# Performance work log

Measured on AMD Instinct MI355X. Metric: run time of the kernel, lower is better.

Reference implementation:

```python
import jax, jax.numpy as jnp
import numpy as np

DIM = 768
NUM_HEADS = 12
HEAD_DIM = DIM // NUM_HEADS
HIDDEN = int(DIM * 0.5)  # 384, per Block: hidden_features = int(dim * 0.5)
SCALE = HEAD_DIM ** 0.5  # NOTE: source multiplies by sqrt(head_dim) (qk_scale=None path)


def setup_inputs() -> dict:
    key = jax.random.key(0)
    ks = jax.random.split(key, 10)
    s = 0.02
    return {
        "x": jax.random.normal(ks[0], (8, 1024, DIM), dtype=jnp.float32),
        "ln1_w": jnp.ones((DIM,), jnp.float32),
        "ln1_b": jnp.zeros((DIM,), jnp.float32),
        "ln2_w": jnp.ones((DIM,), jnp.float32),
        "ln2_b": jnp.zeros((DIM,), jnp.float32),
        "w_qkv": jax.random.normal(ks[1], (DIM, 3 * DIM), jnp.float32) * s,  # no bias (qkv_bias=None)
        "w_proj": jax.random.normal(ks[2], (DIM, DIM), jnp.float32) * s,    # no bias (qkv_bias=None)
        "w_fc1": jax.random.normal(ks[3], (DIM, HIDDEN), jnp.float32) * s,
        "b_fc1": jnp.zeros((HIDDEN,), jnp.float32),
        "w_fc2": jax.random.normal(ks[4], (HIDDEN, DIM), jnp.float32) * s,
        "b_fc2": jnp.zeros((DIM,), jnp.float32),
    }


def _layernorm(x, w, b, eps=1e-5):
    mu = jnp.mean(x, axis=-1, keepdims=True)
    var = jnp.mean(jnp.square(x - mu), axis=-1, keepdims=True)
    return (x - mu) * jax.lax.rsqrt(var + eps) * w + b


def reference(x, ln1_w, ln1_b, ln2_w, ln2_b, w_qkv, w_proj, w_fc1, b_fc1, w_fc2, b_fc2):
    B, N, C = x.shape
    # --- attention branch (pre-norm) ---
    h = _layernorm(x, ln1_w, ln1_b)
    qkv = h @ w_qkv  # [B,N,3C]
    qkv = qkv.reshape(B, N, 3, NUM_HEADS, HEAD_DIM)
    q = jnp.transpose(qkv[:, :, 0], (0, 2, 1, 3))  # [B,H,N,D]
    k = jnp.transpose(qkv[:, :, 1], (0, 2, 1, 3))
    v = jnp.transpose(qkv[:, :, 2], (0, 2, 1, 3))
    attn = jnp.einsum("bhnd,bhmd->bhnm", q, k) * SCALE
    attn = jax.nn.softmax(attn, axis=-1)
    out = jnp.einsum("bhnm,bhmd->bhnd", attn, v)
    out = jnp.transpose(out, (0, 2, 1, 3)).reshape(B, N, C)
    x = x + out @ w_proj
    # --- MLP branch (pre-norm) ---
    h = _layernorm(x, ln2_w, ln2_b)
    h = jax.nn.gelu(h @ w_fc1 + b_fc1, approximate=False)
    x = x + (h @ w_fc2 + b_fc2)
    return x
```

## Files before the change

kernel.cpp:

```cpp
#include <hip/hip_runtime.h>
#include <hip/hip_bf16.h>
#include <math.h>

#define DIM 768
#define NHEAD 12
#define HD 64
#define HIDDEN 384
#define BATCH 8
#define SEQ 1024
#define ROWS (BATCH*SEQ)
#define CHUNKB 4
#define CHUNKR (CHUNKB*SEQ)

typedef short bf16x8 __attribute__((ext_vector_type(8)));
typedef short bf16x4 __attribute__((ext_vector_type(4)));
typedef float f32x4 __attribute__((ext_vector_type(4)));
typedef unsigned short u16;
typedef unsigned int u32;

__device__ __forceinline__ u16 f2bs(float f) {
    unsigned int u = __float_as_uint(f);
    unsigned int r = (u + 0x7FFFu + ((u >> 16) & 1u)) >> 16;
    return (u16)r;
}

__device__ __forceinline__ u32 packbf2(float a, float b) {
    __hip_bfloat162 h = __float22bfloat162_rn(make_float2(a, b));
    u32 r;
    __builtin_memcpy(&r, &h, 4);
    return r;
}

__device__ __forceinline__ void gld16(const u16* g, u16* l) {
    __builtin_amdgcn_global_load_lds(
        (const __attribute__((address_space(1))) unsigned int*)g,
        (__attribute__((address_space(3))) unsigned int*)l, 16, 0, 0);
}

__global__ __launch_bounds__(256) void wtrans(const float* __restrict__ W,
                                              u16* __restrict__ Wt, int K, int N) {
    __shared__ float tile[32][33];
    int n0 = blockIdx.x * 32, k0 = blockIdx.y * 32;
    int tx = threadIdx.x & 31, ty = threadIdx.x >> 5;
#pragma unroll
    for (int i = 0; i < 4; i++)
        tile[ty + i * 8][tx] = W[(long)(k0 + ty + i * 8) * N + n0 + tx];
    __syncthreads();
#pragma unroll
    for (int i = 0; i < 4; i++)
        Wt[(long)(n0 + ty + i * 8) * K + k0 + tx] = f2bs(tile[tx][ty + i * 8]);
}

__global__ __launch_bounds__(256) void lnorm(const float* __restrict__ X,
                                             const float* __restrict__ w,
                                             const float* __restrict__ b,
                                             u16* __restrict__ Y) {
    int row = blockIdx.x;
    const float* xr = X + (long)row * DIM;
    int t = threadIdx.x;
    float v0 = xr[t], v1 = xr[t + 256], v2 = xr[t + 512];
    float s = v0 + v1 + v2;
    float s2 = v0 * v0 + v1 * v1 + v2 * v2;
    for (int off = 1; off < 64; off <<= 1) {
        s  += __shfl_xor(s,  off, 64);
        s2 += __shfl_xor(s2, off, 64);
    }
    __shared__ float ss[4], ss2[4];
    int wid = t >> 6;
    if ((t & 63) == 0) { ss[wid] = s; ss2[wid] = s2; }
    __syncthreads();
    s  = ss[0] + ss[1] + ss[2] + ss[3];
    s2 = ss2[0] + ss2[1] + ss2[2] + ss2[3];
    float mu = s * (1.0f / DIM);
    float var = s2 * (1.0f / DIM) - mu * mu;
    float rstd = rsqrtf(var + 1e-5f);
    u16* yr = Y + (long)row * DIM;
    yr[t]       = f2bs((v0 - mu) * rstd * w[t]       + b[t]);
    yr[t + 256] = f2bs((v1 - mu) * rstd * w[t + 256] + b[t + 256]);
    yr[t + 512] = f2bs((v2 - mu) * rstd * w[t + 512] + b[t + 512]);
}

template <int BM, int BN, int EPI>
__global__ __launch_bounds__(256) void gemm_bt(const u16* __restrict__ A,
                                               const u16* __restrict__ Bt,
                                               int M, int N, int K,
                                               u16* __restrict__ Cb,
                                               float* __restrict__ Cf,
                                               const float* __restrict__ resid,
                                               const float* __restrict__ bias) {
    constexpr int MB = BM / 32, NB = BN / 32;
    __shared__ u16 As[BM * 64];
    __shared__ u16 Bs[BN * 64];
    int m0 = blockIdx.y * BM;
    int n0 = blockIdx.x * BN;
    int t = threadIdx.x;
    int lane = t & 63, w = t >> 6;
    int quad = lane >> 4, l16 = lane & 15;
    int wr = w >> 1, wc = w & 1;
    int lr = lane >> 3, lc = lane & 7;
    int sc = (lc ^ lr) * 8;
    int x7 = l16 & 7;

    f32x4 acc[MB][NB];
#pragma unroll
    for (int mb = 0; mb < MB; mb++)
#pragma unroll
        for (int nb = 0; nb < NB; nb++) acc[mb][nb] = (f32x4){0.f, 0.f, 0.f, 0.f};

    for (int kt = 0; kt < K; kt += 64) {
        __syncthreads();
#pragma unroll
        for (int i = 0; i < BM / 32; i++) {
            int rb = i * 32 + w * 8;
            gld16(&A[(long)(m0 + rb + lr) * K + kt + sc], &As[rb * 64]);
        }
#pragma unroll
        for (int i = 0; i < BN / 32; i++) {
            int rb = i * 32 + w * 8;
            gld16(&Bt[(long)(n0 + rb + lr) * K + kt + sc], &Bs[rb * 64]);
        }
        __syncthreads();
#pragma unroll
        for (int kh = 0; kh < 2; kh++) {
            bf16x8 af[MB], bfr[NB];
#pragma unroll
            for (int mb = 0; mb < MB; mb++)
                af[mb] = *(const bf16x8*)&As[(wr * (BM / 2) + mb * 16 + l16) * 64 +
                                             (((kh * 4 + quad) ^ x7) * 8)];
#pragma unroll
            for (int nb = 0; nb < NB; nb++)
                bfr[nb] = *(const bf16x8*)&Bs[(wc * (BN / 2) + nb * 16 + l16) * 64 +
                                              (((kh * 4 + quad) ^ x7) * 8)];
#pragma unroll
            for (int mb = 0; mb < MB; mb++)
#pragma unroll
                for (int nb = 0; nb < NB; nb++)
                    acc[mb][nb] = __builtin_amdgcn_mfma_f32_16x16x32_bf16(af[mb], bfr[nb], acc[mb][nb], 0, 0, 0);
        }
    }

    int mbase = m0 + wr * (BM / 2), nbase = n0 + wc * (BN / 2);
#pragma unroll
    for (int mb = 0; mb < MB; mb++)
#pragma unroll
        for (int nb = 0; nb < NB; nb++) {
            int r0 = mbase + mb * 16 + quad * 4;
            int c = nbase + nb * 16 + l16;
#pragma unroll
            for (int r = 0; r < 4; r++) {
                float v = acc[mb][nb][r];
                long idx = (long)(r0 + r) * N + c;
                if (EPI == 0) {
                    Cb[idx] = f2bs(v);
                } else if (EPI == 1) {
                    Cf[idx] = resid[idx] + v;
                } else if (EPI == 2) {
                    float xg = v + bias[c];
                    Cb[idx] = f2bs(xg * 0.5f * (1.0f + erff(xg * 0.70710678118f)));
                } else {
                    Cf[idx] = resid[idx] + v + bias[c];
                }
            }
        }
}

__global__ __launch_bounds__(256, 4) void attn(const u16* __restrict__ QKV, u16* __restrict__ O) {
    __shared__ u16 Ks[2][64 * 64];
    __shared__ u16 Vs[2][64 * 72];
    int lin = blockIdx.x;
    int cpx = gridDim.x >> 3;
    int l = (lin & 7) * cpx + (lin >> 3);
    int q0 = (l & 15) * 64;
    int hb = l >> 4;
    int h = hb % NHEAD;
    int b = hb / NHEAD;
    int t = threadIdx.x;
    int lane = t & 63, w = t >> 6;
    int quad = lane >> 4, l16 = lane & 15;
    int x7 = l16 & 7;

    const long rs = 3 * DIM;
    const u16* base = QKV + (long)b * SEQ * rs;

    bf16x8 qf0, qf1;
    {
        int qrow = q0 + w * 16 + l16;
        qf0 = *(const bf16x8*)&base[(long)qrow * rs + h * 64 + quad * 8];
        qf1 = *(const bf16x8*)&base[(long)qrow * rs + h * 64 + 32 + quad * 8];
    }

    f32x4 o[4];
#pragma unroll
    for (int dt = 0; dt < 4; dt++) o[dt] = (f32x4){0.f, 0.f, 0.f, 0.f};
    float m_run = -1e30f;
    float l_run = 0.f;
    const float L2E8 = 11.54156032f;

    int lr = lane >> 3, lc = lane & 7;
    int sc = (lc ^ lr) * 8;
    const u16* kA = &base[(long)(w * 16 + lr) * rs + DIM + h * 64 + sc];
    const u16* kB = kA + (long)8 * rs;
    int vc = t & 31, vo = t >> 5;
    const u16* vptr = &base[(long)(2 * vc) * rs + 2 * DIM + h * 64 + vo * 8];
    const long kstep = (long)64 * rs;

    bf16x8 vp0, vp1;
    gld16(kA, &Ks[0][(w * 16) * 64]);
    gld16(kB, &Ks[0][(w * 16 + 8) * 64]);
    kA += kstep; kB += kstep;
    vp0 = *(const bf16x8*)&vptr[0];
    vp1 = *(const bf16x8*)&vptr[rs];
    vptr += kstep;
#pragma unroll
    for (int j = 0; j < 8; j++) {
        u32 pk = (u32)(u16)vp0[j] | ((u32)(u16)vp1[j] << 16);
        *(u32*)&Vs[0][(vo * 8 + j) * 72 + 2 * vc] = pk;
    }
    vp0 = *(const bf16x8*)&vptr[0];
    vp1 = *(const bf16x8*)&vptr[rs];
    vptr += kstep;
    __syncthreads();

    for (int it = 0; it < SEQ / 64; it++) {
        int cur = it & 1;
        if (it < SEQ / 64 - 1) {
            int nb = cur ^ 1;
            gld16(kA, &Ks[nb][(w * 16) * 64]);
            gld16(kB, &Ks[nb][(w * 16 + 8) * 64]);
            kA += kstep; kB += kstep;
#pragma unroll
            for (int j = 0; j < 8; j++) {
                u32 pk = (u32)(u16)vp0[j] | ((u32)(u16)vp1[j] << 16);
                *(u32*)&Vs[nb][(vo * 8 + j) * 72 + 2 * vc] = pk;
            }
            if (it < SEQ / 64 - 2) {
                vp0 = *(const bf16x8*)&vptr[0];
                vp1 = *(const bf16x8*)&vptr[rs];
                vptr += kstep;
            }
        }

        f32x4 s[4];
#pragma unroll
        for (int jb = 0; jb < 4; jb++) {
            int row = jb * 16 + l16;
            bf16x8 kf0 = *(const bf16x8*)&Ks[cur][row * 64 + ((quad ^ x7) * 8)];
            bf16x8 kf1 = *(const bf16x8*)&Ks[cur][row * 64 + (((4 + quad) ^ x7) * 8)];
            f32x4 z = (f32x4){0.f, 0.f, 0.f, 0.f};
            z = __builtin_amdgcn_mfma_f32_16x16x32_bf16(kf0, qf0, z, 0, 0, 0);
            z = __builtin_amdgcn_mfma_f32_16x16x32_bf16(kf1, qf1, z, 0, 0, 0);
            s[jb] = z;
        }

        f32x4 mx = __builtin_elementwise_max(__builtin_elementwise_max(s[0], s[1]),
                                             __builtin_elementwise_max(s[2], s[3]));
        float m1 = fmaxf(fmaxf(mx[0], mx[1]), fmaxf(mx[2], mx[3]));
        m1 = fmaxf(m1, __shfl_xor(m1, 16, 64));
        m1 = fmaxf(m1, __shfl_xor(m1, 32, 64));

        float mn = m_run;
        int resc = __any(m1 > mn + 1.0f);
        if (resc) mn = fmaxf(mn, m1);
        float mn8 = mn * L2E8;
        f32x4 cmul = {L2E8, L2E8, L2E8, L2E8};
        f32x4 cadd = {-mn8, -mn8, -mn8, -mn8};
#pragma unroll
        for (int jb = 0; jb < 4; jb++) {
            f32x4 e = s[jb] * cmul + cadd;
            e[0] = exp2f(e[0]); e[1] = exp2f(e[1]);
            e[2] = exp2f(e[2]); e[3] = exp2f(e[3]);
            s[jb] = e;
        }
        f32x4 sv = (s[0] + s[1]) + (s[2] + s[3]);
        float rsum = (sv[0] + sv[1]) + (sv[2] + sv[3]);
        rsum += __shfl_xor(rsum, 16, 64);
        rsum += __shfl_xor(rsum, 32, 64);

        if (resc) {
            float alpha = exp2f((m_run - mn) * L2E8);
            m_run = mn;
            float a0 = __shfl(alpha, quad * 4 + 0, 16);
            float a1 = __shfl(alpha, quad * 4 + 1, 16);
            float a2 = __shfl(alpha, quad * 4 + 2, 16);
            float a3 = __shfl(alpha, quad * 4 + 3, 16);
#pragma unroll
            for (int dt = 0; dt < 4; dt++) {
                o[dt][0] *= a0; o[dt][1] *= a1;
                o[dt][2] *= a2; o[dt][3] *= a3;
            }
            l_run = l_run * alpha + rsum;
        } else {
            l_run += rsum;
        }

#pragma unroll
        for (int jb = 0; jb < 4; jb++) {
            union { u32 u[2]; bf16x4 v; } pc;
            pc.u[0] = packbf2(s[jb][0], s[jb][1]);
            pc.u[1] = packbf2(s[jb][2], s[jb][3]);
            bf16x4 pf = pc.v;
#pragma unroll
            for (int dt = 0; dt < 4; dt++) {
                bf16x4 vf = *(const bf16x4*)&Vs[cur][(dt * 16 + l16) * 72 + jb * 16 + quad * 4];
                o[dt] = __builtin_amdgcn_mfma_f32_16x16x16bf16_1k(pf, vf, o[dt], 0, 0, 0);
            }
        }

        if (it < SEQ / 64 - 1) __syncthreads();
    }

    {
        float l0 = __shfl(l_run, quad * 4 + 0, 16);
        float l1 = __shfl(l_run, quad * 4 + 1, 16);
        float l2 = __shfl(l_run, quad * 4 + 2, 16);
        float l3 = __shfl(l_run, quad * 4 + 3, 16);
        u16* orow = O + ((long)(b * SEQ + q0 + w * 16)) * DIM + h * 64;
#pragma unroll
        for (int dt = 0; dt < 4; dt++) {
            u32 p01 = packbf2(o[dt][0] / l0, o[dt][1] / l1);
            u32 p23 = packbf2(o[dt][2] / l2, o[dt][3] / l3);
            int cidx = dt * 16 + l16;
            orow[(long)(quad * 4 + 0) * DIM + cidx] = (u16)p01;
            orow[(long)(quad * 4 + 1) * DIM + cidx] = (u16)(p01 >> 16);
            orow[(long)(quad * 4 + 2) * DIM + cidx] = (u16)p23;
            orow[(long)(quad * 4 + 3) * DIM + cidx] = (u16)(p23 >> 16);
        }
    }
}

extern "C" void kernel_launch(void* const* d_in, const int* in_sizes, int n_in,
                              void* d_out, int out_size, void* d_ws, size_t ws_size,
                              hipStream_t stream) {
    const float* x     = (const float*)d_in[0];
    const float* ln1w  = (const float*)d_in[1];
    const float* ln1b  = (const float*)d_in[2];
    const float* ln2w  = (const float*)d_in[3];
    const float* ln2b  = (const float*)d_in[4];
    const float* wqkv  = (const float*)d_in[5];
    const float* wproj = (const float*)d_in[6];
    const float* wfc1  = (const float*)d_in[7];
    const float* bfc1  = (const float*)d_in[8];
    const float* wfc2  = (const float*)d_in[9];
    const float* bfc2  = (const float*)d_in[10];
    float* out = (float*)d_out;

    char* ws = (char*)d_ws;
    size_t off = 0;
    auto alloc = [&](size_t bytes) {
        void* p = ws + off;
        off = (off + bytes + 255) & ~(size_t)255;
        return p;
    };
    u16* wt_qkv  = (u16*)alloc((size_t)3 * DIM * DIM * 2);
    u16* wt_proj = (u16*)alloc((size_t)DIM * DIM * 2);
    u16* wt_fc1  = (u16*)alloc((size_t)HIDDEN * DIM * 2);
    u16* wt_fc2  = (u16*)alloc((size_t)DIM * HIDDEN * 2);
    u16* hbuf    = (u16*)alloc((size_t)ROWS * DIM * 2);
    u16* gbuf    = (u16*)alloc((size_t)ROWS * HIDDEN * 2);
    size_t qkv_bytes = (size_t)ROWS * 3 * DIM * 2;
    u16* qkvfull = (off + qkv_bytes + 1024 <= ws_size) ? (u16*)alloc(qkv_bytes) : nullptr;

    wtrans<<<dim3(3 * DIM / 32, DIM / 32), 256, 0, stream>>>(wqkv, wt_qkv, DIM, 3 * DIM);
    wtrans<<<dim3(DIM / 32, DIM / 32), 256, 0, stream>>>(wproj, wt_proj, DIM, DIM);
    wtrans<<<dim3(HIDDEN / 32, DIM / 32), 256, 0, stream>>>(wfc1, wt_fc1, DIM, HIDDEN);
    wtrans<<<dim3(DIM / 32, HIDDEN / 32), 256, 0, stream>>>(wfc2, wt_fc2, HIDDEN, DIM);

    lnorm<<<ROWS, 256, 0, stream>>>(x, ln1w, ln1b, hbuf);

    if (qkvfull) {
        gemm_bt<128, 128, 0><<<dim3(3 * DIM / 128, ROWS / 128), 256, 0, stream>>>(
            hbuf, wt_qkv, ROWS, 3 * DIM, DIM, qkvfull, nullptr, nullptr, nullptr);
        attn<<<(SEQ / 64) * NHEAD * BATCH, 256, 0, stream>>>(qkvfull, hbuf);
    } else {
        u16* qd = (u16*)d_out;
        for (int c = 0; c < ROWS / CHUNKR; c++) {
            const u16* hA = hbuf + (size_t)c * CHUNKR * DIM;
            gemm_bt<128, 128, 0><<<dim3(3 * DIM / 128, CHUNKR / 128), 256, 0, stream>>>(
                hA, wt_qkv, CHUNKR, 3 * DIM, DIM, qd, nullptr, nullptr, nullptr);
            attn<<<(SEQ / 64) * NHEAD * CHUNKB, 256, 0, stream>>>(
                qd, hbuf + (size_t)c * CHUNKR * DIM);
        }
    }

    gemm_bt<128, 64, 1><<<dim3(DIM / 64, ROWS / 128), 256, 0, stream>>>(
        hbuf, wt_proj, ROWS, DIM, DIM, nullptr, out, x, nullptr);

    lnorm<<<ROWS, 256, 0, stream>>>(out, ln2w, ln2b, hbuf);

    gemm_bt<64, 64, 2><<<dim3(HIDDEN / 64, ROWS / 64), 256, 0, stream>>>(
        hbuf, wt_fc1, ROWS, HIDDEN, DIM, gbuf, nullptr, nullptr, bfc1);

    gemm_bt<128, 64, 3><<<dim3(DIM / 64, ROWS / 128), 256, 0, stream>>>(
        gbuf, wt_fc2, ROWS, DIM, HIDDEN, nullptr, out, out, bfc2);
}
```

Measured before the change: 293.2 us.

## Use 128-query attention blocks with 8 waves sharing K/V tiles; fuse weight transposes

The attention kernel now launches 512-thread blocks, each covering 128 query rows with 8 waves. Every K/V tile staged in shared memory is reused by twice as many queries, and each thread loads half as much per tile. The four weight-transpose launches are merged into one kernel that picks its matrix from the block index, saving launch overhead. The trade-off is half as many attention blocks and a higher occupancy target (launch bounds 512,6), which may constrain registers.

```diff
diff --git a/kernel.cpp b/kernel.cpp
--- a/kernel.cpp
+++ b/kernel.cpp
@@ -37,10 +37,18 @@
         (__attribute__((address_space(3))) unsigned int*)l, 16, 0, 0);
 }
 
-__global__ __launch_bounds__(256) void wtrans(const float* __restrict__ W,
-                                              u16* __restrict__ Wt, int K, int N) {
+__global__ __launch_bounds__(256) void wtrans4(const float* __restrict__ W0, u16* __restrict__ T0,
+                                               const float* __restrict__ W1, u16* __restrict__ T1,
+                                               const float* __restrict__ W2, u16* __restrict__ T2,
+                                               const float* __restrict__ W3, u16* __restrict__ T3) {
     __shared__ float tile[32][33];
-    int n0 = blockIdx.x * 32, k0 = blockIdx.y * 32;
+    int id = blockIdx.x;
+    const float* W; u16* T; int K, N, nt;
+    if (id < 1728)      {            W = W0; T = T0; K = 768; N = 2304; nt = 72; }
+    else if (id < 2304) { id -= 1728; W = W1; T = T1; K = 768; N = 768;  nt = 24; }
+    else if (id < 2592) { id -= 2304; W = W2; T = T2; K = 768; N = 384;  nt = 12; }
+    else                { id -= 2592; W = W3; T = T3; K = 384; N = 768;  nt = 24; }
+    int n0 = (id % nt) * 32, k0 = (id / nt) * 32;
     int tx = threadIdx.x & 31, ty = threadIdx.x >> 5;
 #pragma unroll
     for (int i = 0; i < 4; i++)
@@ -48,7 +56,7 @@
     __syncthreads();
 #pragma unroll
     for (int i = 0; i < 4; i++)
-        Wt[(long)(n0 + ty + i * 8) * K + k0 + tx] = f2bs(tile[tx][ty + i * 8]);
+        T[(long)(n0 + ty + i * 8) * K + k0 + tx] = f2bs(tile[tx][ty + i * 8]);
 }
 
 __global__ __launch_bounds__(256) void lnorm(const float* __restrict__ X,
@@ -164,14 +172,14 @@
         }
 }
 
-__global__ __launch_bounds__(256, 4) void attn(const u16* __restrict__ QKV, u16* __restrict__ O) {
+__global__ __launch_bounds__(512, 6) void attn(const u16* __restrict__ QKV, u16* __restrict__ O) {
     __shared__ u16 Ks[2][64 * 64];
     __shared__ u16 Vs[2][64 * 72];
     int lin = blockIdx.x;
     int cpx = gridDim.x >> 3;
     int l = (lin & 7) * cpx + (lin >> 3);
-    int q0 = (l & 15) * 64;
-    int hb = l >> 4;
+    int q0 = (l & 7) * 128;
+    int hb = l >> 3;
     int h = hb % NHEAD;
     int b = hb / NHEAD;
     int t = threadIdx.x;
@@ -198,26 +206,24 @@
 
     int lr = lane >> 3, lc = lane & 7;
     int sc = (lc ^ lr) * 8;
-    const u16* kA = &base[(long)(w * 16 + lr) * rs + DIM + h * 64 + sc];
-    const u16* kB = kA + (long)8 * rs;
+    const u16* kA = &base[(long)(w * 8 + lr) * rs + DIM + h * 64 + sc];
     int vc = t & 31, vo = t >> 5;
-    const u16* vptr = &base[(long)(2 * vc) * rs + 2 * DIM + h * 64 + vo * 8];
+    const u16* vptr = &base[(long)(2 * vc) * rs + 2 * DIM + h * 64 + vo * 4];
     const long kstep = (long)64 * rs;
 
-    bf16x8 vp0, vp1;
-    gld16(kA, &Ks[0][(w * 16) * 64]);
-    gld16(kB, &Ks[0][(w * 16 + 8) * 64]);
-    kA += kstep; kB += kstep;
-    vp0 = *(const bf16x8*)&vptr[0];
-    vp1 = *(const bf16x8*)&vptr[rs];
+    bf16x4 vp0, vp1;
+    gld16(kA, &Ks[0][(w * 8) * 64]);
+    kA += kstep;
+    vp0 = *(const bf16x4*)&vptr[0];
+    vp1 = *(const bf16x4*)&vptr[rs];
     vptr += kstep;
 #pragma unroll
-    for (int j = 0; j < 8; j++) {
+    for (int j = 0; j < 4; j++) {
         u32 pk = (u32)(u16)vp0[j] | ((u32)(u16)vp1[j] << 16);
-        *(u32*)&Vs[0][(vo * 8 + j) * 72 + 2 * vc] = pk;
-    }
-    vp0 = *(const bf16x8*)&vptr[0];
-    vp1 = *(const bf16x8*)&vptr[rs];
+        *(u32*)&Vs[0][(vo * 4 + j) * 72 + 2 * vc] = pk;
+    }
+    vp0 = *(const bf16x4*)&vptr[0];
+    vp1 = *(const bf16x4*)&vptr[rs];
     vptr += kstep;
     __syncthreads();
 
@@ -225,17 +231,16 @@
         int cur = it & 1;
         if (it < SEQ / 64 - 1) {
             int nb = cur ^ 1;
-            gld16(kA, &Ks[nb][(w * 16) * 64]);
-            gld16(kB, &Ks[nb][(w * 16 + 8) * 64]);
-            kA += kstep; kB += kstep;
-#pragma unroll
-            for (int j = 0; j < 8; j++) {
+            gld16(kA, &Ks[nb][(w * 8) * 64]);
+            kA += kstep;
+#pragma unroll
+            for (int j = 0; j < 4; j++) {
                 u32 pk = (u32)(u16)vp0[j] | ((u32)(u16)vp1[j] << 16);
-                *(u32*)&Vs[nb][(vo * 8 + j) * 72 + 2 * vc] = pk;
+                *(u32*)&Vs[nb][(vo * 4 + j) * 72 + 2 * vc] = pk;
             }
             if (it < SEQ / 64 - 2) {
-                vp0 = *(const bf16x8*)&vptr[0];
-                vp1 = *(const bf16x8*)&vptr[rs];
+                vp0 = *(const bf16x4*)&vptr[0];
+                vp1 = *(const bf16x4*)&vptr[rs];
                 vptr += kstep;
             }
         }
@@ -360,24 +365,22 @@
     size_t qkv_bytes = (size_t)ROWS * 3 * DIM * 2;
     u16* qkvfull = (off + qkv_bytes + 1024 <= ws_size) ? (u16*)alloc(qkv_bytes) : nullptr;
 
-    wtrans<<<dim3(3 * DIM / 32, DIM / 32), 256, 0, stream>>>(wqkv, wt_qkv, DIM, 3 * DIM);
-    wtrans<<<dim3(DIM / 32, DIM / 32), 256, 0, stream>>>(wproj, wt_proj, DIM, DIM);
-    wtrans<<<dim3(HIDDEN / 32, DIM / 32), 256, 0, stream>>>(wfc1, wt_fc1, DIM, HIDDEN);
-    wtrans<<<dim3(DIM / 32, HIDDEN / 32), 256, 0, stream>>>(wfc2, wt_fc2, HIDDEN, DIM);
+    wtrans4<<<2880, 256, 0, stream>>>(wqkv, wt_qkv, wproj, wt_proj,
+                                      wfc1, wt_fc1, wfc2, wt_fc2);
 
     lnorm<<<ROWS, 256, 0, stream>>>(x, ln1w, ln1b, hbuf);
 
     if (qkvfull) {
         gemm_bt<128, 128, 0><<<dim3(3 * DIM / 128, ROWS / 128), 256, 0, stream>>>(
             hbuf, wt_qkv, ROWS, 3 * DIM, DIM, qkvfull, nullptr, nullptr, nullptr);
-        attn<<<(SEQ / 64) * NHEAD * BATCH, 256, 0, stream>>>(qkvfull, hbuf);
+        attn<<<(SEQ / 128) * NHEAD * BATCH, 512, 0, stream>>>(qkvfull, hbuf);
     } else {
         u16* qd = (u16*)d_out;
         for (int c = 0; c < ROWS / CHUNKR; c++) {
             const u16* hA = hbuf + (size_t)c * CHUNKR * DIM;
             gemm_bt<128, 128, 0><<<dim3(3 * DIM / 128, CHUNKR / 128), 256, 0, stream>>>(
                 hA, wt_qkv, CHUNKR, 3 * DIM, DIM, qd, nullptr, nullptr, nullptr);
-            attn<<<(SEQ / 64) * NHEAD * CHUNKB, 256, 0, stream>>>(
+            attn<<<(SEQ / 128) * NHEAD * CHUNKB, 512, 0, stream>>>(
                 qd, hbuf + (size_t)c * CHUNKR * DIM);
         }
     }
```

Measured after the change: 269.3 us. -8.2%, faster.
